# Kernel tuning notes

Measured on AMD Instinct MI355X. Metric: run time of the kernel, lower is better.

## Reference

```python
import jax, jax.numpy as jnp
import numpy as np

THETA = 10000.0
B, S, D, H = 2, 2048, 1024, 16
DK = D // H


def setup_inputs() -> dict:
    key = jax.random.key(0)
    k1, k2, k3 = jax.random.split(key, 3)
    x = jax.random.normal(k1, (B, S, D), jnp.float32)
    # trunc_normal init approximated by scaled normal (std = 2/(d_k+d_model))
    weight = jax.random.normal(k2, (3, H, DK, D), jnp.float32) * (2.0 / (DK + D))
    wo_weight = jax.random.normal(k3, (D, H * DK), jnp.float32) * (2.0 / (2 * D))
    token_positions = jnp.arange(S, dtype=jnp.int32)
    return {"x": x, "token_positions": token_positions, "weight": weight, "wo_weight": wo_weight}


def _rope(x, cos, sin):
    # x: (..., seq, d_k); rotate interleaved pairs
    x1 = jnp.stack((-x[..., 1::2], x[..., ::2]), axis=-1).reshape(x.shape)
    return x * cos + x1 * sin


def _masked_softmax(scores, mask):
    # matches reference: exp(x - rowmax over ALL entries), zero masked, normalize, zero again
    e = jnp.exp(scores - jnp.max(scores, axis=-1, keepdims=True))
    e = jnp.where(mask, e, 0.0)
    a = e / jnp.sum(e, axis=-1, keepdims=True)
    return jnp.where(mask, a, 0.0)


def reference(x, token_positions, weight, wo_weight):
    dk = weight.shape[2]
    seq_len = x.shape[-2]
    # fused QKV projection: (b, 3, h, s, dk)
    qkv = jnp.einsum('bsd,qhkd->bqhsk', x, weight)
    # RoPE tables from token positions
    pos = token_positions.astype(jnp.float32)[:, None]          # (s, 1)
    kidx = jnp.arange(1, dk // 2 + 1, dtype=jnp.float32)[None]  # (1, dk/2)
    theta = pos / (THETA ** ((2.0 * kidx - 2.0) / dk))          # (s, dk/2)
    cos = jnp.repeat(jnp.cos(theta), 2, axis=-1)                # (s, dk)
    sin = jnp.repeat(jnp.sin(theta), 2, axis=-1)
    q = _rope(qkv[:, 0], cos, sin)   # (b, h, s, dk)
    k = _rope(qkv[:, 1], cos, sin)
    v = qkv[:, 2]
    scores = jnp.einsum('bhqd,bhkd->bhqk', q, k) / jnp.sqrt(jnp.float32(dk))
    mask = jnp.tril(jnp.ones((seq_len, seq_len), dtype=bool))
    att = _masked_softmax(scores, mask)
    out = jnp.einsum('bhqk,bhkd->bhqd', att, v)                 # (b, h, s, dv)
    out = jnp.transpose(out, (0, 2, 1, 3)).reshape(*x.shape[:-1], -1)  # (b, s, h*dv)
    return jnp.einsum('bsi,oi->bso', out, wo_weight)
```

## Files before the change

kernel.cpp:

```cpp
#include <hip/hip_runtime.h>
#include <hip/hip_bf16.h>
#include <math.h>

#define B_   2
#define S_   2048
#define D_   1024
#define H_   16
#define DK_  64
#define NQKV 3072
#define M_   (B_ * S_)

typedef unsigned short u16;
typedef unsigned int   u32;
typedef __attribute__((ext_vector_type(8))) short short8;
typedef __attribute__((ext_vector_type(4))) float f32x4;
typedef __attribute__((ext_vector_type(4))) u16   u16x4;

typedef const __attribute__((address_space(1))) void* gvptr;
typedef __attribute__((address_space(3))) void* lvptr;

__device__ __forceinline__ u16 f2bf(float f) {
  union { float f; u32 u; } v; v.f = f;
  u32 r = v.u + 0x7FFF + ((v.u >> 16) & 1);
  return (u16)(r >> 16);
}
__device__ __forceinline__ float bf2f(u16 h) {
  union { u32 u; float f; } v; v.u = ((u32)h) << 16;
  return v.f;
}

#define MEMFENCE() asm volatile("" ::: "memory")
#define RAW_BARRIER() do { MEMFENCE(); __builtin_amdgcn_s_barrier(); MEMFENCE(); } while (0)

__global__ void rope_table_kernel(const int* __restrict__ pos,
                                  float* __restrict__ ct,
                                  float* __restrict__ st) {
  int idx = blockIdx.x * blockDim.x + threadIdx.x;
  int i = idx & 31;
  int s = idx >> 5;
  if (s >= S_) return;
  double p = (double)pos[s];
  double t = p * pow(10000.0, -(double)i / 32.0);
  ct[idx] = (float)cos(t);
  st[idx] = (float)sin(t);
}

__global__ void cvt_f32_bf16(const float* __restrict__ in, u16* __restrict__ out, int n4) {
  int i = blockIdx.x * 256 + threadIdx.x;
  if (i >= n4) return;
  float4 v = ((const float4*)in)[i];
  u16x4 o;
  o[0] = f2bf(v.x); o[1] = f2bf(v.y); o[2] = f2bf(v.z); o[3] = f2bf(v.w);
  ((u16x4*)out)[i] = o;
}

template<bool OUT_BF16>
__global__ __launch_bounds__(256) void gemm_nt_mfma(const u16* __restrict__ A,
                                                    const u16* __restrict__ Bm,
                                                    void* __restrict__ Cout,
                                                    int Nd, int Kd) {
  __shared__ u16 As[128 * 64];
  __shared__ u16 Bs[128 * 64];
  const int t  = threadIdx.x;
  const int w  = t >> 6, l = t & 63;
  const int g  = l >> 4, ln = l & 15;
  const int wm = w >> 1, wn = w & 1;
  const int m0 = blockIdx.y * 128, n0 = blockIdx.x * 128;

  const f32x4 vzero = {0.f, 0.f, 0.f, 0.f};
  f32x4 acc[4][4];
#pragma unroll
  for (int i = 0; i < 4; ++i)
#pragma unroll
    for (int j = 0; j < 4; ++j) acc[i][j] = vzero;

  for (int k0 = 0; k0 < Kd; k0 += 64) {
    __syncthreads();
#pragma unroll
    for (int p = 0; p < 4; ++p) {
      int c = p * 256 + t;
      int r = c >> 3, sx = (c & 7) ^ (r & 7);
      __builtin_amdgcn_global_load_lds(
          (gvptr)(A + (size_t)(m0 + r) * Kd + k0 + sx * 8),
          (lvptr)(&As[(p * 256 + w * 64) * 8]), 16, 0, 0);
      __builtin_amdgcn_global_load_lds(
          (gvptr)(Bm + (size_t)(n0 + r) * Kd + k0 + sx * 8),
          (lvptr)(&Bs[(p * 256 + w * 64) * 8]), 16, 0, 0);
    }
    __syncthreads();

#pragma unroll
    for (int ks = 0; ks < 2; ++ks) {
      short8 af[4], bf[4];
#pragma unroll
      for (int i = 0; i < 4; ++i) {
        int ra = wm * 64 + i * 16 + ln;
        af[i] = *(const short8*)&As[ra * 64 + (((ks * 4 + g) ^ (ra & 7)) * 8)];
        int rb = wn * 64 + i * 16 + ln;
        bf[i] = *(const short8*)&Bs[rb * 64 + (((ks * 4 + g) ^ (rb & 7)) * 8)];
      }
#pragma unroll
      for (int i = 0; i < 4; ++i)
#pragma unroll
        for (int j = 0; j < 4; ++j)
          acc[i][j] = __builtin_amdgcn_mfma_f32_16x16x32_bf16(af[i], bf[j], acc[i][j], 0, 0, 0);
    }
  }

#pragma unroll
  for (int i = 0; i < 4; ++i)
#pragma unroll
    for (int j = 0; j < 4; ++j)
#pragma unroll
      for (int r = 0; r < 4; ++r) {
        size_t row = (size_t)(m0 + wm * 64 + i * 16 + g * 4 + r);
        size_t col = (size_t)(n0 + wn * 64 + j * 16 + ln);
        if (OUT_BF16) ((u16*)Cout)[row * Nd + col] = f2bf(acc[i][j][r]);
        else          ((float*)Cout)[row * Nd + col] = acc[i][j][r];
      }
}

__global__ void rope_bf16_kernel(u16* __restrict__ qkvb,
                                 const float* __restrict__ ct,
                                 const float* __restrict__ st) {
  int tid = blockIdx.x * 256 + threadIdx.x;
  int p4   = (tid & 7) * 4;
  int h    = (tid >> 3) & 15;
  int part = (tid >> 7) & 1;
  int row  = tid >> 8;
  int s    = row & (S_ - 1);
  float4 c4 = *(const float4*)&ct[s * 32 + p4];
  float4 s4 = *(const float4*)&st[s * 32 + p4];
  u16* p = qkvb + (size_t)row * NQKV + part * 1024 + h * 64 + p4 * 2;
  u16 v[8];
  *(uint4*)v = *(const uint4*)p;
  float x0, x1;
  x0 = bf2f(v[0]); x1 = bf2f(v[1]);
  v[0] = f2bf(x0 * c4.x - x1 * s4.x); v[1] = f2bf(x1 * c4.x + x0 * s4.x);
  x0 = bf2f(v[2]); x1 = bf2f(v[3]);
  v[2] = f2bf(x0 * c4.y - x1 * s4.y); v[3] = f2bf(x1 * c4.y + x0 * s4.y);
  x0 = bf2f(v[4]); x1 = bf2f(v[5]);
  v[4] = f2bf(x0 * c4.z - x1 * s4.z); v[5] = f2bf(x1 * c4.z + x0 * s4.z);
  x0 = bf2f(v[6]); x1 = bf2f(v[7]);
  v[6] = f2bf(x0 * c4.w - x1 * s4.w); v[7] = f2bf(x1 * c4.w + x0 * s4.w);
  *(uint4*)p = *(uint4*)v;
}

__global__ __launch_bounds__(256) void v_transpose_kernel(const u16* __restrict__ qkvb,
                                                          u16* __restrict__ Vt) {
  __shared__ u16 tile[64][72];
  const int t = threadIdx.x;
  const int s0 = blockIdx.x * 64, h = blockIdx.y, b = blockIdx.z;
  {
    int r = t >> 2, cs = (t & 3) * 16;
    const u16* src = qkvb + (size_t)(b * S_ + s0 + r) * NQKV + 2048 + h * 64 + cs;
    u16 v[16];
    *(uint4*)&v[0] = *(const uint4*)src;
    *(uint4*)&v[8] = *(const uint4*)(src + 8);
#pragma unroll
    for (int j = 0; j < 16; ++j) tile[cs + j][r] = v[j];
  }
  __syncthreads();
  {
    int d = t >> 2, ss = (t & 3) * 16;
    u16 o[16];
#pragma unroll
    for (int j = 0; j < 16; ++j) o[j] = tile[d][ss + j];
    u16* dst = Vt + ((size_t)(b * H_ + h) * 64 + d) * S_ + s0 + ss;
    *(uint4*)&dst[0] = *(uint4*)&o[0];
    *(uint4*)&dst[8] = *(uint4*)&o[8];
  }
}

__global__ __launch_bounds__(256) void attn_mfma(const u16* __restrict__ qkvb,
                                                 const u16* __restrict__ Vt,
                                                 u16* __restrict__ attb) {
  __shared__ u16 Ks[2][64 * 64];
  __shared__ u16 Vs[2][64 * 64];
  __shared__ u16 Ps[4][16 * 64];
  const int t = threadIdx.x;
  const int w = t >> 6, l = t & 63;
  const int g = l >> 4, ln = l & 15;
  const int h = blockIdx.y, b = blockIdx.z;
  const size_t bS = (size_t)b * S_;
  const u16* Kbase = qkvb + bS * NQKV + D_ + h * 64;
  const u16* Vbase = Vt + (size_t)(b * H_ + h) * 64 * S_;

  auto stage = [&](int buf, int k0) {
#pragma unroll
    for (int p = 0; p < 2; ++p) {
      int c = p * 256 + t;
      int r = c >> 3, sx = (c & 7) ^ (r & 7);
      __builtin_amdgcn_global_load_lds(
          (gvptr)(Kbase + (size_t)(k0 + r) * NQKV + sx * 8),
          (lvptr)(&Ks[buf][(p * 256 + w * 64) * 8]), 16, 0, 0);
      __builtin_amdgcn_global_load_lds(
          (gvptr)(Vbase + (size_t)r * S_ + k0 + sx * 8),
          (lvptr)(&Vs[buf][(p * 256 + w * 64) * 8]), 16, 0, 0);
    }
  };

  const f32x4 vzero = {0.f, 0.f, 0.f, 0.f};

#pragma unroll 1
  for (int half = 0; half < 2; ++half) {
    const int tq = (half == 0) ? (31 - blockIdx.x) : blockIdx.x;
    const int q0 = tq * 64;
    const int nt = tq + 1;
    const int qg = q0 + w * 16 + ln;

    short8 qf[2];
    {
      const u16* qrow = qkvb + (bS + q0 + w * 16 + ln) * NQKV + h * 64;
      qf[0] = *(const short8*)(qrow + g * 8);
      qf[1] = *(const short8*)(qrow + 32 + g * 8);
    }

    f32x4 o[4];
#pragma unroll
    for (int dt = 0; dt < 4; ++dt) o[dt] = vzero;
    float mrun = -INFINITY, lrun = 0.f;

    int cur = 0;
    stage(0, 0);

#pragma unroll 1
    for (int kt = 0; kt < nt; ++kt) {
      const int k0 = kt * 64;
      if (kt + 1 < nt) {
        stage(cur ^ 1, k0 + 64);
        asm volatile("s_waitcnt vmcnt(4)" ::: "memory");
      } else {
        asm volatile("s_waitcnt vmcnt(0)" ::: "memory");
      }
      RAW_BARRIER();

      f32x4 sacc[4];
#pragma unroll
      for (int st = 0; st < 4; ++st) sacc[st] = vzero;
      __builtin_amdgcn_s_setprio(1);
#pragma unroll
      for (int st = 0; st < 4; ++st) {
        const int kr = st * 16 + ln;
#pragma unroll
        for (int ks = 0; ks < 2; ++ks) {
          short8 kf = *(const short8*)&Ks[cur][kr * 64 + (((ks * 4 + g) ^ (kr & 7)) * 8)];
          sacc[st] = __builtin_amdgcn_mfma_f32_16x16x32_bf16(kf, qf[ks], sacc[st], 0, 0, 0);
        }
      }
      __builtin_amdgcn_s_setprio(0);

      float tmax = -INFINITY;
      if (kt == nt - 1) {
#pragma unroll
        for (int st = 0; st < 4; ++st)
#pragma unroll
          for (int r = 0; r < 4; ++r) {
            int key = k0 + st * 16 + g * 4 + r;
            float sv = sacc[st][r] * 0.125f;
            sv = (key <= qg) ? sv : -INFINITY;
            sacc[st][r] = sv;
            tmax = fmaxf(tmax, sv);
          }
      } else {
#pragma unroll
        for (int st = 0; st < 4; ++st)
#pragma unroll
          for (int r = 0; r < 4; ++r) {
            float sv = sacc[st][r] * 0.125f;
            sacc[st][r] = sv;
            tmax = fmaxf(tmax, sv);
          }
      }
      tmax = fmaxf(tmax, __shfl_xor(tmax, 16));
      tmax = fmaxf(tmax, __shfl_xor(tmax, 32));
      float mnew = fmaxf(mrun, tmax);
      float al = 1.f;
      if (!__all(tmax <= mrun)) {
        al = __expf(mrun - mnew);
#pragma unroll
        for (int r = 0; r < 4; ++r) {
          float sr = __shfl(al, g * 4 + r);
#pragma unroll
          for (int dt = 0; dt < 4; ++dt) o[dt][r] *= sr;
        }
      } else {
        mnew = mrun;
      }
      float lsum = 0.f;
#pragma unroll
      for (int st = 0; st < 4; ++st) {
        u16x4 pk;
#pragma unroll
        for (int r = 0; r < 4; ++r) {
          float pe = __expf(sacc[st][r] - mnew);
          lsum += pe;
          pk[r] = f2bf(pe);
        }
        *(u16x4*)&Ps[w][ln * 64 + ((st * 16 + g * 4) ^ ((ln & 7) << 3))] = pk;
      }
      lsum += __shfl_xor(lsum, 16);
      lsum += __shfl_xor(lsum, 32);
      lrun = lrun * al + lsum;
      mrun = mnew;

      __builtin_amdgcn_s_setprio(1);
#pragma unroll
      for (int ks = 0; ks < 2; ++ks) {
        short8 pf = *(const short8*)&Ps[w][ln * 64 + (((ks * 4 + g) ^ (ln & 7)) * 8)];
#pragma unroll
        for (int dt = 0; dt < 4; ++dt) {
          const int dr = dt * 16 + ln;
          short8 vf = *(const short8*)&Vs[cur][dr * 64 + (((ks * 4 + g) ^ (dr & 7)) * 8)];
          o[dt] = __builtin_amdgcn_mfma_f32_16x16x32_bf16(pf, vf, o[dt], 0, 0, 0);
        }
      }
      __builtin_amdgcn_s_setprio(0);

      asm volatile("s_waitcnt lgkmcnt(0)" ::: "memory");
      RAW_BARRIER();
      cur ^= 1;
    }

    float linv = 1.f / lrun;
#pragma unroll
    for (int r = 0; r < 4; ++r) {
      float ir = __shfl(linv, g * 4 + r);
      size_t row = bS + q0 + w * 16 + g * 4 + r;
#pragma unroll
      for (int dt = 0; dt < 4; ++dt)
        attb[row * D_ + h * 64 + dt * 16 + ln] = f2bf(o[dt][r] * ir);
    }
    asm volatile("s_waitcnt vmcnt(0)" ::: "memory");
  }
}

extern "C" void kernel_launch(void* const* d_in, const int* in_sizes, int n_in,
                              void* d_out, int out_size, void* d_ws, size_t ws_size,
                              hipStream_t stream) {
  (void)in_sizes; (void)n_in; (void)out_size; (void)ws_size;
  const float* x   = (const float*)d_in[0];
  const int*   pos = (const int*)d_in[1];
  const float* w   = (const float*)d_in[2];
  const float* wo  = (const float*)d_in[3];
  float* out = (float*)d_out;

  u16* qkvb = (u16*)d_ws;
  u16* Vt   = qkvb + (size_t)M_ * NQKV;
  u16* attb = Vt + (size_t)B_ * H_ * 64 * S_;
  u16* xb   = attb + (size_t)M_ * D_;
  u16* wb   = xb + (size_t)M_ * D_;
  u16* wob  = wb + (size_t)NQKV * D_;
  float* ct = (float*)(wob + (size_t)D_ * D_);
  float* st = ct + S_ * 32;

  rope_table_kernel<<<(S_ * 32) / 256, 256, 0, stream>>>(pos, ct, st);

  cvt_f32_bf16<<<(M_ * D_ / 4) / 256, 256, 0, stream>>>(x, xb, M_ * D_ / 4);
  cvt_f32_bf16<<<(NQKV * D_ / 4) / 256, 256, 0, stream>>>(w, wb, NQKV * D_ / 4);
  cvt_f32_bf16<<<(D_ * D_ / 4) / 256, 256, 0, stream>>>(wo, wob, D_ * D_ / 4);

  gemm_nt_mfma<true><<<dim3(NQKV / 128, M_ / 128), 256, 0, stream>>>(xb, wb, qkvb, NQKV, D_);

  rope_bf16_kernel<<<(M_ * 256) / 256, 256, 0, stream>>>(qkvb, ct, st);
  v_transpose_kernel<<<dim3(S_ / 64, H_, B_), 256, 0, stream>>>(qkvb, Vt);

  attn_mfma<<<dim3(16, H_, B_), 256, 0, stream>>>(qkvb, Vt, attb);

  gemm_nt_mfma<false><<<dim3(D_ / 128, M_ / 128), 256, 0, stream>>>(attb, wob, out, D_, D_);
}
```

Measured before the change: 211.4 us.

## Fuse RoPE into QKV GEMM epilogue, merge converts, restructure attention to 512 threads

Applies RoPE inside the QKV GEMM epilogue using an interleaved cos/sin table and lane shuffles, which removes the separate rope kernel and its read-modify-write pass. The three f32-to-bf16 converts become one launch. The attention kernel moves to 128-query blocks with 8 waves, triple-buffered K/V staging, and Q pre-scaled by log2e/sqrt(dk) so softmax can use exp2. P stays in registers through packed bf16 converts instead of going through LDS, and max rescaling is lazy with a threshold of 8. The larger blocks halve the grid and add fully masked tile skipping per wave, at some risk to occupancy and load balance.

New measurement: 208.1 us. Within noise of the previous version (-1.6%).

```diff
diff --git a/kernel.cpp b/kernel.cpp
--- a/kernel.cpp
+++ b/kernel.cpp
@@ -19,6 +19,14 @@
 typedef const __attribute__((address_space(1))) void* gvptr;
 typedef __attribute__((address_space(3))) void* lvptr;
 
+#define QSCALE 0.18033688011f
+
+#if __has_builtin(__builtin_amdgcn_exp2f)
+#define EXP2F(x) __builtin_amdgcn_exp2f(x)
+#else
+#define EXP2F(x) __expf(0.69314718056f * (x))
+#endif
+
 __device__ __forceinline__ u16 f2bf(float f) {
   union { float f; u32 u; } v; v.f = f;
   u32 r = v.u + 0x7FFF + ((v.u >> 16) & 1);
@@ -28,36 +36,49 @@
   union { u32 u; float f; } v; v.u = ((u32)h) << 16;
   return v.f;
 }
+__device__ __forceinline__ u32 cvtpk_bf16(float lo, float hi) {
+  u32 r;
+  asm("v_cvt_pk_bf16_f32 %0, %1, %2" : "=v"(r) : "v"(lo), "v"(hi));
+  return r;
+}
 
 #define MEMFENCE() asm volatile("" ::: "memory")
 #define RAW_BARRIER() do { MEMFENCE(); __builtin_amdgcn_s_barrier(); MEMFENCE(); } while (0)
 
-__global__ void rope_table_kernel(const int* __restrict__ pos,
-                                  float* __restrict__ ct,
-                                  float* __restrict__ st) {
-  int idx = blockIdx.x * blockDim.x + threadIdx.x;
+#define SWZ(r) ((((r) & 7) ^ ((((r) >> 3) & 1) << 2)))
+
+__global__ void rope_cs_kernel(const int* __restrict__ pos,
+                               float2* __restrict__ cs) {
+  int idx = blockIdx.x * 256 + threadIdx.x;
   int i = idx & 31;
   int s = idx >> 5;
-  if (s >= S_) return;
   double p = (double)pos[s];
   double t = p * pow(10000.0, -(double)i / 32.0);
-  ct[idx] = (float)cos(t);
-  st[idx] = (float)sin(t);
-}
-
-__global__ void cvt_f32_bf16(const float* __restrict__ in, u16* __restrict__ out, int n4) {
+  cs[idx] = make_float2((float)cos(t), (float)sin(t));
+}
+
+#define N4X (M_ * D_ / 4)
+#define N4W (NQKV * D_ / 4)
+#define N4WO (D_ * D_ / 4)
+__global__ void cvt_all_kernel(const float* __restrict__ x,
+                               const float* __restrict__ w,
+                               const float* __restrict__ wo,
+                               u16* __restrict__ dst) {
   int i = blockIdx.x * 256 + threadIdx.x;
-  if (i >= n4) return;
-  float4 v = ((const float4*)in)[i];
+  float4 v;
+  if (i < N4X)            v = ((const float4*)x)[i];
+  else if (i < N4X + N4W) v = ((const float4*)w)[i - N4X];
+  else                    v = ((const float4*)wo)[i - (N4X + N4W)];
   u16x4 o;
   o[0] = f2bf(v.x); o[1] = f2bf(v.y); o[2] = f2bf(v.z); o[3] = f2bf(v.w);
-  ((u16x4*)out)[i] = o;
-}
-
-template<bool OUT_BF16>
+  ((u16x4*)dst)[i] = o;
+}
+
+template<bool OUT_BF16, bool ROPE>
 __global__ __launch_bounds__(256) void gemm_nt_mfma(const u16* __restrict__ A,
                                                     const u16* __restrict__ Bm,
                                                     void* __restrict__ Cout,
+                                                    const float2* __restrict__ cstab,
                                                     int Nd, int Kd) {
   __shared__ u16 As[128 * 64];
   __shared__ u16 Bs[128 * 64];
@@ -107,43 +128,37 @@
     }
   }
 
-#pragma unroll
-  for (int i = 0; i < 4; ++i)
-#pragma unroll
-    for (int j = 0; j < 4; ++j)
+  if (ROPE && n0 < 2048) {
+#pragma unroll
+    for (int i = 0; i < 4; ++i)
 #pragma unroll
       for (int r = 0; r < 4; ++r) {
-        size_t row = (size_t)(m0 + wm * 64 + i * 16 + g * 4 + r);
-        size_t col = (size_t)(n0 + wn * 64 + j * 16 + ln);
-        if (OUT_BF16) ((u16*)Cout)[row * Nd + col] = f2bf(acc[i][j][r]);
-        else          ((float*)Cout)[row * Nd + col] = acc[i][j][r];
+        int rowi = m0 + wm * 64 + i * 16 + g * 4 + r;
+        int srow = rowi & (S_ - 1);
+#pragma unroll
+        for (int j = 0; j < 4; ++j) {
+          int dk = j * 16 + ln;
+          float2 cs = cstab[srow * 32 + (dk >> 1)];
+          float v = acc[i][j][r];
+          float p = __shfl_xor(v, 1);
+          float sn = (ln & 1) ? cs.y : -cs.y;
+          float rot = fmaf(p, sn, v * cs.x);
+          ((u16*)Cout)[(size_t)rowi * Nd + n0 + wn * 64 + j * 16 + ln] = f2bf(rot);
+        }
       }
-}
-
-__global__ void rope_bf16_kernel(u16* __restrict__ qkvb,
-                                 const float* __restrict__ ct,
-                                 const float* __restrict__ st) {
-  int tid = blockIdx.x * 256 + threadIdx.x;
-  int p4   = (tid & 7) * 4;
-  int h    = (tid >> 3) & 15;
-  int part = (tid >> 7) & 1;
-  int row  = tid >> 8;
-  int s    = row & (S_ - 1);
-  float4 c4 = *(const float4*)&ct[s * 32 + p4];
-  float4 s4 = *(const float4*)&st[s * 32 + p4];
-  u16* p = qkvb + (size_t)row * NQKV + part * 1024 + h * 64 + p4 * 2;
-  u16 v[8];
-  *(uint4*)v = *(const uint4*)p;
-  float x0, x1;
-  x0 = bf2f(v[0]); x1 = bf2f(v[1]);
-  v[0] = f2bf(x0 * c4.x - x1 * s4.x); v[1] = f2bf(x1 * c4.x + x0 * s4.x);
-  x0 = bf2f(v[2]); x1 = bf2f(v[3]);
-  v[2] = f2bf(x0 * c4.y - x1 * s4.y); v[3] = f2bf(x1 * c4.y + x0 * s4.y);
-  x0 = bf2f(v[4]); x1 = bf2f(v[5]);
-  v[4] = f2bf(x0 * c4.z - x1 * s4.z); v[5] = f2bf(x1 * c4.z + x0 * s4.z);
-  x0 = bf2f(v[6]); x1 = bf2f(v[7]);
-  v[6] = f2bf(x0 * c4.w - x1 * s4.w); v[7] = f2bf(x1 * c4.w + x0 * s4.w);
-  *(uint4*)p = *(uint4*)v;
+  } else {
+#pragma unroll
+    for (int i = 0; i < 4; ++i)
+#pragma unroll
+      for (int j = 0; j < 4; ++j)
+#pragma unroll
+        for (int r = 0; r < 4; ++r) {
+          size_t row = (size_t)(m0 + wm * 64 + i * 16 + g * 4 + r);
+          size_t col = (size_t)(n0 + wn * 64 + j * 16 + ln);
+          if (OUT_BF16) ((u16*)Cout)[row * Nd + col] = f2bf(acc[i][j][r]);
+          else          ((float*)Cout)[row * Nd + col] = acc[i][j][r];
+        }
+  }
 }
 
 __global__ __launch_bounds__(256) void v_transpose_kernel(const u16* __restrict__ qkvb,
@@ -172,12 +187,11 @@
   }
 }
 
-__global__ __launch_bounds__(256) void attn_mfma(const u16* __restrict__ qkvb,
+__global__ __launch_bounds__(512) void attn_mfma(const u16* __restrict__ qkvb,
                                                  const u16* __restrict__ Vt,
                                                  u16* __restrict__ attb) {
-  __shared__ u16 Ks[2][64 * 64];
-  __shared__ u16 Vs[2][64 * 64];
-  __shared__ u16 Ps[4][16 * 64];
+  __shared__ u16 Ks[3][64 * 64];
+  __shared__ u16 Vs[3][64 * 64];
   const int t = threadIdx.x;
   const int w = t >> 6, l = t & 63;
   const int g = l >> 4, ln = l & 15;
@@ -186,34 +200,37 @@
   const u16* Kbase = qkvb + bS * NQKV + D_ + h * 64;
   const u16* Vbase = Vt + (size_t)(b * H_ + h) * 64 * S_;
 
+  const int sr = t >> 3;
+  const int ssx = (t & 7) ^ SWZ(sr);
   auto stage = [&](int buf, int k0) {
-#pragma unroll
-    for (int p = 0; p < 2; ++p) {
-      int c = p * 256 + t;
-      int r = c >> 3, sx = (c & 7) ^ (r & 7);
-      __builtin_amdgcn_global_load_lds(
-          (gvptr)(Kbase + (size_t)(k0 + r) * NQKV + sx * 8),
-          (lvptr)(&Ks[buf][(p * 256 + w * 64) * 8]), 16, 0, 0);
-      __builtin_amdgcn_global_load_lds(
-          (gvptr)(Vbase + (size_t)r * S_ + k0 + sx * 8),
-          (lvptr)(&Vs[buf][(p * 256 + w * 64) * 8]), 16, 0, 0);
-    }
+    __builtin_amdgcn_global_load_lds(
+        (gvptr)(Kbase + (size_t)(k0 + sr) * NQKV + ssx * 8),
+        (lvptr)(&Ks[buf][w * 512]), 16, 0, 0);
+    __builtin_amdgcn_global_load_lds(
+        (gvptr)(Vbase + (size_t)sr * S_ + k0 + ssx * 8),
+        (lvptr)(&Vs[buf][w * 512]), 16, 0, 0);
   };
 
   const f32x4 vzero = {0.f, 0.f, 0.f, 0.f};
 
 #pragma unroll 1
   for (int half = 0; half < 2; ++half) {
-    const int tq = (half == 0) ? (31 - blockIdx.x) : blockIdx.x;
-    const int q0 = tq * 64;
-    const int nt = tq + 1;
+    const int tq = (half == 0) ? (15 - blockIdx.x) : blockIdx.x;
+    const int q0 = tq * 128;
+    const int nt = 2 * tq + 2;
     const int qg = q0 + w * 16 + ln;
+    const int wqmax = q0 + w * 16 + 15;
 
     short8 qf[2];
     {
       const u16* qrow = qkvb + (bS + q0 + w * 16 + ln) * NQKV + h * 64;
       qf[0] = *(const short8*)(qrow + g * 8);
       qf[1] = *(const short8*)(qrow + 32 + g * 8);
+#pragma unroll
+      for (int kx = 0; kx < 2; ++kx)
+#pragma unroll
+        for (int e = 0; e < 8; ++e)
+          qf[kx][e] = (short)f2bf(bf2f((u16)qf[kx][e]) * QSCALE);
     }
 
     f32x4 o[4];
@@ -221,105 +238,108 @@
     for (int dt = 0; dt < 4; ++dt) o[dt] = vzero;
     float mrun = -INFINITY, lrun = 0.f;
 
+    stage(0, 0);
+    stage(1, 64);
     int cur = 0;
-    stage(0, 0);
 
 #pragma unroll 1
     for (int kt = 0; kt < nt; ++kt) {
       const int k0 = kt * 64;
-      if (kt + 1 < nt) {
-        stage(cur ^ 1, k0 + 64);
+      if (kt + 2 < nt) {
+        int pre = cur + 2; if (pre >= 3) pre -= 3;
+        stage(pre, k0 + 128);
         asm volatile("s_waitcnt vmcnt(4)" ::: "memory");
+      } else if (kt + 1 < nt) {
+        asm volatile("s_waitcnt vmcnt(2)" ::: "memory");
       } else {
         asm volatile("s_waitcnt vmcnt(0)" ::: "memory");
       }
       RAW_BARRIER();
 
-      f32x4 sacc[4];
-#pragma unroll
-      for (int st = 0; st < 4; ++st) sacc[st] = vzero;
-      __builtin_amdgcn_s_setprio(1);
-#pragma unroll
-      for (int st = 0; st < 4; ++st) {
-        const int kr = st * 16 + ln;
-#pragma unroll
-        for (int ks = 0; ks < 2; ++ks) {
-          short8 kf = *(const short8*)&Ks[cur][kr * 64 + (((ks * 4 + g) ^ (kr & 7)) * 8)];
-          sacc[st] = __builtin_amdgcn_mfma_f32_16x16x32_bf16(kf, qf[ks], sacc[st], 0, 0, 0);
-        }
+      if (k0 <= wqmax) {
+        f32x4 sacc[4];
+#pragma unroll
+        for (int st = 0; st < 4; ++st) sacc[st] = vzero;
+        __builtin_amdgcn_s_setprio(1);
+#pragma unroll
+        for (int st = 0; st < 4; ++st) {
+          const int pr = ((ln >> 2) << 3) + ((st & 1) << 2) + (ln & 3) + ((st >> 1) << 5);
+#pragma unroll
+          for (int ks = 0; ks < 2; ++ks) {
+            short8 kf = *(const short8*)&Ks[cur][pr * 64 + (((ks * 4 + g) ^ SWZ(pr)) * 8)];
+            sacc[st] = __builtin_amdgcn_mfma_f32_16x16x32_bf16(kf, qf[ks], sacc[st], 0, 0, 0);
+          }
+        }
+        __builtin_amdgcn_s_setprio(0);
+
+        float tmax = -INFINITY;
+        if (k0 + 63 > q0 + w * 16) {
+#pragma unroll
+          for (int st = 0; st < 4; ++st)
+#pragma unroll
+            for (int r = 0; r < 4; ++r) {
+              int key = k0 + g * 8 + ((st & 1) << 2) + r + ((st >> 1) << 5);
+              if (key > qg) sacc[st][r] = -INFINITY;
+              tmax = fmaxf(tmax, sacc[st][r]);
+            }
+        } else {
+#pragma unroll
+          for (int st = 0; st < 4; ++st)
+#pragma unroll
+            for (int r = 0; r < 4; ++r) tmax = fmaxf(tmax, sacc[st][r]);
+        }
+        tmax = fmaxf(tmax, __shfl_xor(tmax, 16));
+        tmax = fmaxf(tmax, __shfl_xor(tmax, 32));
+        float al = 1.f, mnew = mrun;
+        if (!__all(tmax <= mrun + 8.0f)) {
+          mnew = fmaxf(mrun, tmax);
+          al = EXP2F(mrun - mnew);
+#pragma unroll
+          for (int r = 0; r < 4; ++r) {
+            float srs = __shfl(al, g * 4 + r);
+#pragma unroll
+            for (int dt = 0; dt < 4; ++dt) o[dt][r] *= srs;
+          }
+        }
+        float lsum = 0.f;
+#pragma unroll
+        for (int st = 0; st < 4; ++st)
+#pragma unroll
+          for (int r = 0; r < 4; ++r) {
+            float pe = EXP2F(sacc[st][r] - mnew);
+            sacc[st][r] = pe;
+            lsum += pe;
+          }
+        lsum += __shfl_xor(lsum, 16);
+        lsum += __shfl_xor(lsum, 32);
+        lrun = lrun * al + lsum;
+        mrun = mnew;
+
+        union { u32 u[4]; short8 v; } pa[2];
+        pa[0].u[0] = cvtpk_bf16(sacc[0][0], sacc[0][1]);
+        pa[0].u[1] = cvtpk_bf16(sacc[0][2], sacc[0][3]);
+        pa[0].u[2] = cvtpk_bf16(sacc[1][0], sacc[1][1]);
+        pa[0].u[3] = cvtpk_bf16(sacc[1][2], sacc[1][3]);
+        pa[1].u[0] = cvtpk_bf16(sacc[2][0], sacc[2][1]);
+        pa[1].u[1] = cvtpk_bf16(sacc[2][2], sacc[2][3]);
+        pa[1].u[2] = cvtpk_bf16(sacc[3][0], sacc[3][1]);
+        pa[1].u[3] = cvtpk_bf16(sacc[3][2], sacc[3][3]);
+
+        __builtin_amdgcn_s_setprio(1);
+#pragma unroll
+        for (int ks = 0; ks < 2; ++ks)
+#pragma unroll
+          for (int dt = 0; dt < 4; ++dt) {
+            const int dr = dt * 16 + ln;
+            short8 vf = *(const short8*)&Vs[cur][dr * 64 + (((ks * 4 + g) ^ SWZ(dr)) * 8)];
+            o[dt] = __builtin_amdgcn_mfma_f32_16x16x32_bf16(pa[ks].v, vf, o[dt], 0, 0, 0);
+          }
+        __builtin_amdgcn_s_setprio(0);
       }
-      __builtin_amdgcn_s_setprio(0);
-
-      float tmax = -INFINITY;
-      if (kt == nt - 1) {
-#pragma unroll
-        for (int st = 0; st < 4; ++st)
-#pragma unroll
-          for (int r = 0; r < 4; ++r) {
-            int key = k0 + st * 16 + g * 4 + r;
-            float sv = sacc[st][r] * 0.125f;
-            sv = (key <= qg) ? sv : -INFINITY;
-            sacc[st][r] = sv;
-            tmax = fmaxf(tmax, sv);
-          }
-      } else {
-#pragma unroll
-        for (int st = 0; st < 4; ++st)
-#pragma unroll
-          for (int r = 0; r < 4; ++r) {
-            float sv = sacc[st][r] * 0.125f;
-            sacc[st][r] = sv;
-            tmax = fmaxf(tmax, sv);
-          }
-      }
-      tmax = fmaxf(tmax, __shfl_xor(tmax, 16));
-      tmax = fmaxf(tmax, __shfl_xor(tmax, 32));
-      float mnew = fmaxf(mrun, tmax);
-      float al = 1.f;
-      if (!__all(tmax <= mrun)) {
-        al = __expf(mrun - mnew);
-#pragma unroll
-        for (int r = 0; r < 4; ++r) {
-          float sr = __shfl(al, g * 4 + r);
-#pragma unroll
-          for (int dt = 0; dt < 4; ++dt) o[dt][r] *= sr;
-        }
-      } else {
-        mnew = mrun;
-      }
-      float lsum = 0.f;
-#pragma unroll
-      for (int st = 0; st < 4; ++st) {
-        u16x4 pk;
-#pragma unroll
-        for (int r = 0; r < 4; ++r) {
-          float pe = __expf(sacc[st][r] - mnew);
-          lsum += pe;
-          pk[r] = f2bf(pe);
-        }
-        *(u16x4*)&Ps[w][ln * 64 + ((st * 16 + g * 4) ^ ((ln & 7) << 3))] = pk;
-      }
-      lsum += __shfl_xor(lsum, 16);
-      lsum += __shfl_xor(lsum, 32);
-      lrun = lrun * al + lsum;
-      mrun = mnew;
-
-      __builtin_amdgcn_s_setprio(1);
-#pragma unroll
-      for (int ks = 0; ks < 2; ++ks) {
-        short8 pf = *(const short8*)&Ps[w][ln * 64 + (((ks * 4 + g) ^ (ln & 7)) * 8)];
-#pragma unroll
-        for (int dt = 0; dt < 4; ++dt) {
-          const int dr = dt * 16 + ln;
-          short8 vf = *(const short8*)&Vs[cur][dr * 64 + (((ks * 4 + g) ^ (dr & 7)) * 8)];
-          o[dt] = __builtin_amdgcn_mfma_f32_16x16x32_bf16(pf, vf, o[dt], 0, 0, 0);
-        }
-      }
-      __builtin_amdgcn_s_setprio(0);
 
       asm volatile("s_waitcnt lgkmcnt(0)" ::: "memory");
       RAW_BARRIER();
-      cur ^= 1;
+      cur = (cur == 2) ? 0 : cur + 1;
     }
 
     float linv = 1.f / lrun;
@@ -351,21 +371,19 @@
   u16* xb   = attb + (size_t)M_ * D_;
   u16* wb   = xb + (size_t)M_ * D_;
   u16* wob  = wb + (size_t)NQKV * D_;
-  float* ct = (float*)(wob + (size_t)D_ * D_);
-  float* st = ct + S_ * 32;
-
-  rope_table_kernel<<<(S_ * 32) / 256, 256, 0, stream>>>(pos, ct, st);
-
-  cvt_f32_bf16<<<(M_ * D_ / 4) / 256, 256, 0, stream>>>(x, xb, M_ * D_ / 4);
-  cvt_f32_bf16<<<(NQKV * D_ / 4) / 256, 256, 0, stream>>>(w, wb, NQKV * D_ / 4);
-  cvt_f32_bf16<<<(D_ * D_ / 4) / 256, 256, 0, stream>>>(wo, wob, D_ * D_ / 4);
-
-  gemm_nt_mfma<true><<<dim3(NQKV / 128, M_ / 128), 256, 0, stream>>>(xb, wb, qkvb, NQKV, D_);
-
-  rope_bf16_kernel<<<(M_ * 256) / 256, 256, 0, stream>>>(qkvb, ct, st);
+  float2* cstab = (float2*)(wob + (size_t)D_ * D_);
+
+  rope_cs_kernel<<<(S_ * 32) / 256, 256, 0, stream>>>(pos, cstab);
+
+  cvt_all_kernel<<<(N4X + N4W + N4WO) / 256, 256, 0, stream>>>(x, w, wo, xb);
+
+  gemm_nt_mfma<true, true><<<dim3(NQKV / 128, M_ / 128), 256, 0, stream>>>(
+      xb, wb, qkvb, cstab, NQKV, D_);
+
   v_transpose_kernel<<<dim3(S_ / 64, H_, B_), 256, 0, stream>>>(qkvb, Vt);
 
-  attn_mfma<<<dim3(16, H_, B_), 256, 0, stream>>>(qkvb, Vt, attb);
-
-  gemm_nt_mfma<false><<<dim3(D_ / 128, M_ / 128), 256, 0, stream>>>(attb, wob, out, D_, D_);
-}
+  attn_mfma<<<dim3(8, H_, B_), 512, 0, stream>>>(qkvb, Vt, attb);
+
+  gemm_nt_mfma<false, false><<<dim3(D_ / 128, M_ / 128), 256, 0, stream>>>(
+      attb, wob, out, nullptr, D_, D_);
+}
```
